# Optimization experiments

Hardware: AMD Instinct MI355X
Metric: run time of the kernel (lower is better)

The kernel has to match this reference:

```python
import jax, jax.numpy as jnp
import numpy as np

B, S, D, F, E, K = 4, 2048, 768, 3072, 8, 2
LB_W, Z_W = 0.01, 0.001


def setup_inputs() -> dict:
    key = jax.random.key(0)
    ks = jax.random.split(key, 6)
    x = jax.random.normal(ks[0], (B, S, D), dtype=jnp.float32)
    Wr = jax.random.truncated_normal(ks[1], -2.0, 2.0, (D, E), dtype=jnp.float32) * 0.02
    W1 = jax.random.normal(ks[2], (E, D, F), dtype=jnp.float32) * (1.0 / np.sqrt(D))
    b1 = jnp.zeros((E, F), dtype=jnp.float32)
    W2 = jax.random.normal(ks[3], (E, F, D), dtype=jnp.float32) * (1.0 / np.sqrt(F))
    b2 = jnp.zeros((E, D), dtype=jnp.float32)
    return {"x": x, "Wr": Wr, "W1": W1, "b1": b1, "W2": W2, "b2": b2}


def reference(x, Wr, W1, b1, W2, b2):
    # Router
    router_logits = jnp.einsum('bsd,de->bse', x, Wr)            # [B,S,E]
    router_probs = jax.nn.softmax(router_logits, axis=-1)
    top_k_probs, top_k_idx = jax.lax.top_k(router_probs, K)     # [B,S,K]
    top_k_probs = top_k_probs / (jnp.sum(top_k_probs, axis=-1, keepdims=True) + 1e-8)

    # Auxiliary losses
    expert_usage = jnp.mean(router_probs, axis=(0, 1))          # [E]
    mean_usage = jnp.mean(expert_usage)
    var_usage = jnp.mean(jnp.square(expert_usage - mean_usage))
    lb_loss = var_usage / (mean_usage * mean_usage + 1e-8) * jnp.float32(E)
    z_loss = jnp.mean(jnp.square(jax.nn.logsumexp(router_logits, axis=-1)))

    # Combine weights per expert: sum over top-k slots assigned to expert e
    one_hot = jax.nn.one_hot(top_k_idx, E, dtype=x.dtype)       # [B,S,K,E]
    combine = jnp.sum(one_hot * top_k_probs[..., None], axis=2) # [B,S,E]

    # Expert FFNs (loop over fixed small E, vectorized over tokens)
    output = jnp.zeros_like(x)
    for e in range(E):
        h = jax.nn.gelu(jnp.einsum('bsd,df->bsf', x, W1[e]) + b1[e], approximate=False)
        y = jnp.einsum('bsf,fd->bsd', h, W2[e]) + b2[e]
        output = output + y * combine[..., e:e + 1]

    aux = {"load_balancing_loss": lb_loss * LB_W, "router_z_loss": z_loss * Z_W}
    return output, aux["load_balancing_loss"], aux["router_z_loss"]
```

## Files before the change

### kernel.cpp

```cpp
#include <hip/hip_runtime.h>
#include <cstdint>
#include <cstddef>

#define B_ 4
#define S_ 2048
#define D_ 768
#define F_ 3072
#define E_ 8
#define NTOK (B_*S_)
#define NASSIGN (NTOK*2)
#define RBLK 256
#define FBLK 32
#define MAXTILE 136

typedef unsigned short u16;
typedef __attribute__((ext_vector_type(8))) __bf16 bf16x8;
typedef __attribute__((ext_vector_type(4))) float f32x4;

__device__ __forceinline__ u16 f2bf(float f) {
    unsigned int u = __builtin_bit_cast(unsigned int, f);
    u += 0x7fffu + ((u >> 16) & 1u);
    return (u16)(u >> 16);
}

__device__ __forceinline__ void async16(const void* g, void* l) {
    __builtin_amdgcn_global_load_lds(
        (const __attribute__((address_space(1))) unsigned int*)g,
        (__attribute__((address_space(3))) unsigned int*)l, 16, 0, 0);
}

__device__ __forceinline__ float gelu_f(float v) {
    float z = v * 0.70710678f;
    float a = fabsf(z);
    float t = __builtin_amdgcn_rcpf(1.0f + 0.3275911f * a);
    float poly = t * (0.254829592f + t * (-0.284496736f + t * (1.421413741f +
                 t * (-1.453152027f + t * 1.061405429f))));
    float e = __expf(-z * z);
    float erf_z = copysignf(1.0f - poly * e, z);
    return 0.5f * v * (1.0f + erf_z);
}

__device__ __forceinline__ int xcd_tile(int xcd, int mloc, int nt, int* ok) {
    int q = nt >> 3, r = nt & 7;
    int cntx = q + (xcd < r ? 1 : 0);
    *ok = (mloc < cntx);
    return xcd * q + (xcd < r ? xcd : r) + mloc;
}

__global__ void k_cvt_x(const float* __restrict__ x, u16* __restrict__ xb) {
    int id = blockIdx.x * 256 + threadIdx.x;
    float4 v = ((const float4*)x)[id];
    ushort4 o;
    o.x = f2bf(v.x); o.y = f2bf(v.y); o.z = f2bf(v.z); o.w = f2bf(v.w);
    ((ushort4*)xb)[id] = o;
}

__global__ __launch_bounds__(256) void k_tcvt(const float* __restrict__ in, u16* __restrict__ out, int R, int C) {
    __shared__ u16 t[64][72];
    int e = blockIdx.z;
    int c0 = blockIdx.x * 64, r0 = blockIdx.y * 64;
    int tid = threadIdx.x;
    int sx = tid & 15;
    int sy = tid >> 4;
    const float* ip = in + (size_t)e * R * C + (size_t)(r0 + sy * 4) * C + c0 + sx * 4;
    float4 v0 = *(const float4*)(ip);
    float4 v1 = *(const float4*)(ip + C);
    float4 v2 = *(const float4*)(ip + 2 * (size_t)C);
    float4 v3 = *(const float4*)(ip + 3 * (size_t)C);
    ushort4 o;
    o.x = f2bf(v0.x); o.y = f2bf(v1.x); o.z = f2bf(v2.x); o.w = f2bf(v3.x);
    *(ushort4*)&t[sx * 4 + 0][sy * 4] = o;
    o.x = f2bf(v0.y); o.y = f2bf(v1.y); o.z = f2bf(v2.y); o.w = f2bf(v3.y);
    *(ushort4*)&t[sx * 4 + 1][sy * 4] = o;
    o.x = f2bf(v0.z); o.y = f2bf(v1.z); o.z = f2bf(v2.z); o.w = f2bf(v3.z);
    *(ushort4*)&t[sx * 4 + 2][sy * 4] = o;
    o.x = f2bf(v0.w); o.y = f2bf(v1.w); o.z = f2bf(v2.w); o.w = f2bf(v3.w);
    *(ushort4*)&t[sx * 4 + 3][sy * 4] = o;
    __syncthreads();
    int od = tid & 7;
    int oc = tid >> 3;
    u16* obase = out + (size_t)e * C * R;
    #pragma unroll
    for (int p = 0; p < 2; p++) {
        int c = oc + p * 32;
        *(uint4*)(obase + (size_t)(c0 + c) * R + r0 + od * 8) = *(const uint4*)&t[c][od * 8];
    }
}

__global__ __launch_bounds__(256) void k_router(
    const float* __restrict__ x, const float* __restrict__ Wr,
    float* __restrict__ usage_part, float* __restrict__ z_part,
    int* __restrict__ hist_part,
    int* __restrict__ tk_idx, float* __restrict__ tk_w)
{
    __shared__ float wrt[E_ * D_];
    __shared__ float s_usage[E_];
    __shared__ float s_z;
    __shared__ int   s_hist[E_];
    int tid = threadIdx.x;
    for (int i = tid; i < E_ * D_; i += 256) {
        int d = i >> 3, e = i & 7;
        wrt[e * D_ + d] = Wr[i];
    }
    if (tid < E_) { s_usage[tid] = 0.f; s_hist[tid] = 0; }
    if (tid == 0) s_z = 0.f;
    __syncthreads();

    int w = tid >> 6, lane = tid & 63;
    float u_acc[E_];
    #pragma unroll
    for (int e = 0; e < E_; e++) u_acc[e] = 0.f;
    float z_acc = 0.f;

    for (int it = 0; it < 8; it++) {
        int tok = blockIdx.x * 32 + it * 4 + w;
        float acc[E_];
        #pragma unroll
        for (int e = 0; e < E_; e++) acc[e] = 0.f;
        const float* xr = x + (size_t)tok * D_;
        for (int d = lane; d < D_; d += 64) {
            float xv = xr[d];
            #pragma unroll
            for (int e = 0; e < E_; e++) acc[e] += xv * wrt[e * D_ + d];
        }
        #pragma unroll
        for (int off = 32; off > 0; off >>= 1) {
            #pragma unroll
            for (int e = 0; e < E_; e++) acc[e] += __shfl_down(acc[e], off);
        }
        if (lane == 0) {
            float m = acc[0];
            #pragma unroll
            for (int e = 1; e < E_; e++) m = fmaxf(m, acc[e]);
            float p[E_], s = 0.f;
            #pragma unroll
            for (int e = 0; e < E_; e++) { p[e] = expf(acc[e] - m); s += p[e]; }
            float inv = 1.f / s;
            #pragma unroll
            for (int e = 0; e < E_; e++) { p[e] *= inv; u_acc[e] += p[e]; }
            float lse = m + logf(s);
            z_acc += lse * lse;
            int i1 = 0;
            for (int e = 1; e < E_; e++) if (p[e] > p[i1]) i1 = e;
            int i2 = -1;
            for (int e = 0; e < E_; e++) {
                if (e == i1) continue;
                if (i2 < 0 || p[e] > p[i2]) i2 = e;
            }
            float denom = p[i1] + p[i2] + 1e-8f;
            tk_idx[tok * 2 + 0] = i1; tk_idx[tok * 2 + 1] = i2;
            tk_w[tok * 2 + 0] = p[i1] / denom;
            tk_w[tok * 2 + 1] = p[i2] / denom;
            atomicAdd(&s_hist[i1], 1); atomicAdd(&s_hist[i2], 1);
        }
    }
    if (lane == 0) {
        #pragma unroll
        for (int e = 0; e < E_; e++) atomicAdd(&s_usage[e], u_acc[e]);
        atomicAdd(&s_z, z_acc);
    }
    __syncthreads();
    if (tid < E_) {
        usage_part[blockIdx.x * E_ + tid] = s_usage[tid];
        hist_part[blockIdx.x * E_ + tid]  = s_hist[tid];
    }
    if (tid == 0) z_part[blockIdx.x] = s_z;
}

__global__ __launch_bounds__(256) void k_finalize(
    const float* __restrict__ usage_part, const float* __restrict__ z_part,
    const int* __restrict__ hist_part,
    int* __restrict__ counts, int* __restrict__ offsets,
    int* __restrict__ cursors,
    int* __restrict__ tile_list,
    float* __restrict__ out_scalars)
{
    __shared__ float s_u[E_];
    __shared__ float s_z;
    __shared__ int   s_h[E_];
    int tid = threadIdx.x;
    if (tid < E_) { s_u[tid] = 0.f; s_h[tid] = 0; cursors[tid] = 0; }
    if (tid == 0) s_z = 0.f;
    __syncthreads();

    float u[E_]; int h[E_];
    #pragma unroll
    for (int e = 0; e < E_; e++) { u[e] = usage_part[tid * E_ + e]; h[e] = hist_part[tid * E_ + e]; }
    float z = z_part[tid];
    #pragma unroll
    for (int off = 32; off > 0; off >>= 1) {
        #pragma unroll
        for (int e = 0; e < E_; e++) {
            u[e] += __shfl_down(u[e], off);
            h[e] += __shfl_down(h[e], off);
        }
        z += __shfl_down(z, off);
    }
    if ((tid & 63) == 0) {
        #pragma unroll
        for (int e = 0; e < E_; e++) { atomicAdd(&s_u[e], u[e]); atomicAdd(&s_h[e], h[e]); }
        atomicAdd(&s_z, z);
    }
    __syncthreads();
    if (tid == 0) {
        int o = 0, nt = 0;
        for (int e = 0; e < E_; e++) {
            int c = s_h[e];
            counts[e] = c; offsets[e] = o; o += c;
            for (int m0 = 0; m0 < c; m0 += 128) tile_list[1 + nt++] = (m0 << 8) | e;
        }
        tile_list[0] = nt;
        float uu[E_], mean = 0.f;
        for (int e = 0; e < E_; e++) { uu[e] = s_u[e] / (float)NTOK; mean += uu[e]; }
        mean /= (float)E_;
        float var = 0.f;
        for (int e = 0; e < E_; e++) { float d = uu[e] - mean; var += d * d; }
        var /= (float)E_;
        out_scalars[0] = var / (mean * mean + 1e-8f) * (float)E_ * 0.01f;
        out_scalars[1] = (s_z / (float)NTOK) * 0.001f;
    }
}

__global__ __launch_bounds__(256) void k_fill(
    const int* __restrict__ tk_idx, const float* __restrict__ tk_w,
    const int* __restrict__ offsets, int* __restrict__ cursors,
    int* __restrict__ assign_token, float* __restrict__ assign_weight)
{
    __shared__ int l_cnt[E_];
    __shared__ int l_base[E_];
    int tid = threadIdx.x;
    if (tid < E_) l_cnt[tid] = 0;
    __syncthreads();
    int t = blockIdx.x * 256 + tid;
    int e0 = tk_idx[t * 2 + 0], e1 = tk_idx[t * 2 + 1];
    int r0 = atomicAdd(&l_cnt[e0], 1);
    int r1 = atomicAdd(&l_cnt[e1], 1);
    __syncthreads();
    if (tid < E_) l_base[tid] = atomicAdd(&cursors[tid], l_cnt[tid]);
    __syncthreads();
    int row0 = offsets[e0] + l_base[e0] + r0;
    int row1 = offsets[e1] + l_base[e1] + r1;
    assign_token[row0] = t; assign_weight[row0] = tk_w[t * 2 + 0];
    assign_token[row1] = t; assign_weight[row1] = tk_w[t * 2 + 1];
}

__global__ __launch_bounds__(256) void k_gemm1(
    const u16* __restrict__ xb, const u16* __restrict__ w1t,
    const float* __restrict__ b1,
    const int* __restrict__ counts, const int* __restrict__ offsets,
    const int* __restrict__ tile_list,
    const int* __restrict__ assign_token, u16* __restrict__ h)
{
    int bid = blockIdx.x;
    int xcd = bid & 7;
    int j = bid >> 3;
    int nx = j / 17;
    int mloc = j % 17;
    int nt = tile_list[0];
    int ok;
    int mt = xcd_tile(xcd, mloc, nt, &ok);
    if (!ok) return;
    int packed = tile_list[1 + mt];
    int e = packed & 0xff;
    int m0 = packed >> 8;
    int cnt = counts[e];
    int off = offsets[e];
    int n0 = nx * 128;

    __shared__ __align__(16) u16 SM[16384];
    char* smb = (char*)SM;

    int tid = threadIdx.x;
    int w = tid >> 6, lane = tid & 63;
    int rA = lane >> 2;
    int colk = ((lane & 3) ^ (rA & 3)) * 8;
    int r0 = (w * 2 + 0) * 16 + rA;
    int r1 = (w * 2 + 1) * 16 + rA;

    int c0b = __builtin_amdgcn_readfirstlane((w * 2 + 0) * 1024);
    int c1b = __builtin_amdgcn_readfirstlane((w * 2 + 1) * 1024);

    int g0 = m0 + r0; if (g0 > cnt - 1) g0 = cnt - 1;
    int g1 = m0 + r1; if (g1 > cnt - 1) g1 = cnt - 1;
    const u16* agp0 = xb + (size_t)assign_token[off + g0] * D_ + colk;
    const u16* agp1 = xb + (size_t)assign_token[off + g1] * D_ + colk;
    const u16* bgp0 = w1t + ((size_t)e * F_ + n0 + r0) * D_ + colk;
    const u16* bgp1 = w1t + ((size_t)e * F_ + n0 + r1) * D_ + colk;

    f32x4 acc[4][4];
    #pragma unroll
    for (int i = 0; i < 4; i++)
        #pragma unroll
        for (int j2 = 0; j2 < 4; j2++) acc[i][j2] = (f32x4){0.f, 0.f, 0.f, 0.f};

    int wm = (w >> 1) * 64, wn = (w & 1) * 64;
    int fm = lane & 15;
    int slot = ((lane >> 4) ^ (fm & 3)) * 8;

    #define STAGE1(buf, kk) do { \
        async16(agp0 + (kk), smb + (buf) * 8192 + c0b); \
        async16(agp1 + (kk), smb + (buf) * 8192 + c1b); \
        async16(bgp0 + (kk), smb + 16384 + (buf) * 8192 + c0b); \
        async16(bgp1 + (kk), smb + 16384 + (buf) * 8192 + c1b); \
    } while (0)
    #define COMPUTE1(buf) do { \
        const u16* Ab = SM + (buf) * 4096; \
        const u16* Bb = SM + 8192 + (buf) * 4096; \
        bf16x8 af[4], bfr[4]; \
        _Pragma("unroll") \
        for (int i = 0; i < 4; i++) af[i] = *(const bf16x8*)&Ab[(wm + i * 16 + fm) * 32 + slot]; \
        _Pragma("unroll") \
        for (int j2 = 0; j2 < 4; j2++) bfr[j2] = *(const bf16x8*)&Bb[(wn + j2 * 16 + fm) * 32 + slot]; \
        _Pragma("unroll") \
        for (int i = 0; i < 4; i++) \
            _Pragma("unroll") \
            for (int j2 = 0; j2 < 4; j2++) \
                acc[i][j2] = __builtin_amdgcn_mfma_f32_16x16x32_bf16(af[i], bfr[j2], acc[i][j2], 0, 0, 0); \
    } while (0)

    STAGE1(0, 0);
    __syncthreads();
    for (int kk = 0; kk < D_; kk += 64) {
        STAGE1(1, kk + 32);
        COMPUTE1(0);
        __syncthreads();
        if (kk + 64 < D_) STAGE1(0, kk + 64);
        COMPUTE1(1);
        __syncthreads();
    }
    #undef STAGE1
    #undef COMPUTE1

    int rbase = (lane >> 4) * 4;
    u16* tb = SM + w * 4096;
    float biasv[4];
    #pragma unroll
    for (int j2 = 0; j2 < 4; j2++) biasv[j2] = b1[e * F_ + n0 + wn + j2 * 16 + fm];
    #pragma unroll
    for (int i = 0; i < 4; i++)
        #pragma unroll
        for (int j2 = 0; j2 < 4; j2++)
            #pragma unroll
            for (int r = 0; r < 4; r++) {
                int m_l = i * 16 + rbase + r;
                int f_l = j2 * 16 + fm;
                u16 q = f2bf(gelu_f(acc[i][j2][r] + biasv[j2]));
                tb[m_l * 64 + ((((f_l >> 3) ^ (m_l & 7)) << 3) | (f_l & 7))] = q;
            }
    __syncthreads();
    #pragma unroll
    for (int s = 0; s < 8; s++) {
        int m_l = s * 8 + (lane >> 3);
        int c = lane & 7;
        uint4 vv = *(const uint4*)&tb[m_l * 64 + ((c ^ (m_l & 7)) << 3)];
        int m = m0 + wm + m_l;
        if (m < cnt)
            *(uint4*)&h[(size_t)(off + m) * F_ + n0 + wn + c * 8] = vv;
    }
}

__global__ __launch_bounds__(256) void k_gemm2(
    const u16* __restrict__ h, const u16* __restrict__ w2t,
    const float* __restrict__ b2,
    const int* __restrict__ counts, const int* __restrict__ offsets,
    const int* __restrict__ tile_list,
    const int* __restrict__ assign_token, const float* __restrict__ assign_weight,
    float* __restrict__ out)
{
    int bid = blockIdx.x;
    int xcd = bid & 7;
    int j = bid >> 3;
    int mloc = j / 12;
    int rem = j % 12;
    int nx = rem % 6;
    int kh = rem / 6;
    int nt = tile_list[0];
    int ok;
    int mt = xcd_tile(xcd, mloc, nt, &ok);
    if (!ok) return;
    int packed = tile_list[1 + mt];
    int e = packed & 0xff;
    int m0 = packed >> 8;
    int cnt = counts[e];
    int off = offsets[e];
    int n0 = nx * 128;
    int kbase = kh * (F_ / 2);
    int kend = kbase + F_ / 2;

    __shared__ __align__(16) u16 SM[16384];
    char* smb = (char*)SM;

    int tid = threadIdx.x;
    int w = tid >> 6, lane = tid & 63;
    int rA = lane >> 2;
    int colk = ((lane & 3) ^ (rA & 3)) * 8;
    int r0 = (w * 2 + 0) * 16 + rA;
    int r1 = (w * 2 + 1) * 16 + rA;

    int c0b = __builtin_amdgcn_readfirstlane((w * 2 + 0) * 1024);
    int c1b = __builtin_amdgcn_readfirstlane((w * 2 + 1) * 1024);

    const u16* agp0 = h + (size_t)(off + m0 + r0) * F_ + colk;
    const u16* agp1 = h + (size_t)(off + m0 + r1) * F_ + colk;
    const u16* bgp0 = w2t + ((size_t)e * D_ + n0 + r0) * F_ + colk;
    const u16* bgp1 = w2t + ((size_t)e * D_ + n0 + r1) * F_ + colk;

    f32x4 acc[4][4];
    #pragma unroll
    for (int i = 0; i < 4; i++)
        #pragma unroll
        for (int j2 = 0; j2 < 4; j2++) acc[i][j2] = (f32x4){0.f, 0.f, 0.f, 0.f};

    int wm = (w >> 1) * 64, wn = (w & 1) * 64;
    int fm = lane & 15;
    int slot = ((lane >> 4) ^ (fm & 3)) * 8;

    #define STAGE2(buf, kk) do { \
        async16(agp0 + (kk), smb + (buf) * 8192 + c0b); \
        async16(agp1 + (kk), smb + (buf) * 8192 + c1b); \
        async16(bgp0 + (kk), smb + 16384 + (buf) * 8192 + c0b); \
        async16(bgp1 + (kk), smb + 16384 + (buf) * 8192 + c1b); \
    } while (0)
    #define COMPUTE2(buf) do { \
        const u16* Ab = SM + (buf) * 4096; \
        const u16* Bb = SM + 8192 + (buf) * 4096; \
        bf16x8 af[4], bfr[4]; \
        _Pragma("unroll") \
        for (int i = 0; i < 4; i++) af[i] = *(const bf16x8*)&Ab[(wm + i * 16 + fm) * 32 + slot]; \
        _Pragma("unroll") \
        for (int j2 = 0; j2 < 4; j2++) bfr[j2] = *(const bf16x8*)&Bb[(wn + j2 * 16 + fm) * 32 + slot]; \
        _Pragma("unroll") \
        for (int i = 0; i < 4; i++) \
            _Pragma("unroll") \
            for (int j2 = 0; j2 < 4; j2++) \
                acc[i][j2] = __builtin_amdgcn_mfma_f32_16x16x32_bf16(af[i], bfr[j2], acc[i][j2], 0, 0, 0); \
    } while (0)

    STAGE2(0, kbase);
    __syncthreads();
    for (int kk = kbase; kk < kend; kk += 64) {
        STAGE2(1, kk + 32);
        COMPUTE2(0);
        __syncthreads();
        if (kk + 64 < kend) STAGE2(0, kk + 64);
        COMPUTE2(1);
        __syncthreads();
    }
    #undef STAGE2
    #undef COMPUTE2

    int rbase = (lane >> 4) * 4;
    float biasv[4];
    #pragma unroll
    for (int j2 = 0; j2 < 4; j2++)
        biasv[j2] = (kh == 0) ? b2[e * D_ + n0 + wn + j2 * 16 + fm] : 0.f;
    #pragma unroll
    for (int i = 0; i < 4; i++)
        #pragma unroll
        for (int r = 0; r < 4; r++) {
            int m = m0 + wm + i * 16 + rbase + r;
            if (m < cnt) {
                int t = assign_token[off + m];
                float wg = assign_weight[off + m];
                float* orow = out + (size_t)t * D_ + n0 + wn + fm;
                #pragma unroll
                for (int j2 = 0; j2 < 4; j2++)
                    unsafeAtomicAdd(orow + j2 * 16, (acc[i][j2][r] + biasv[j2]) * wg);
            }
        }
}

extern "C" void kernel_launch(void* const* d_in, const int* in_sizes, int n_in,
                              void* d_out, int out_size, void* d_ws, size_t ws_size,
                              hipStream_t stream)
{
    const float* x  = (const float*)d_in[0];
    const float* Wr = (const float*)d_in[1];
    const float* W1 = (const float*)d_in[2];
    const float* b1 = (const float*)d_in[3];
    const float* W2 = (const float*)d_in[4];
    const float* b2 = (const float*)d_in[5];
    float* out = (float*)d_out;

    char* base = (char*)d_ws;
    size_t o = 0;
    auto alloc = [&](size_t bytes) {
        char* r = base + o;
        o += (bytes + 255) & ~(size_t)255;
        return r;
    };
    int*   counts        = (int*)  alloc(E_ * 4);
    int*   cursors       = (int*)  alloc(E_ * 4);
    int*   offsets       = (int*)  alloc(E_ * 4);
    int*   tile_list     = (int*)  alloc(256 * 4);
    float* usage_part    = (float*)alloc((size_t)RBLK * E_ * 4);
    float* z_part        = (float*)alloc((size_t)RBLK * 4);
    int*   hist_part     = (int*)  alloc((size_t)RBLK * E_ * 4);
    int*   tk_idx        = (int*)  alloc((size_t)NTOK * 2 * 4);
    float* tk_w          = (float*)alloc((size_t)NTOK * 2 * 4);
    int*   assign_token  = (int*)  alloc((size_t)NASSIGN * 4);
    float* assign_weight = (float*)alloc((size_t)NASSIGN * 4);
    u16*   xb            = (u16*)  alloc((size_t)NTOK * D_ * 2);
    u16*   w1t           = (u16*)  alloc((size_t)E_ * F_ * D_ * 2);
    u16*   w2t           = (u16*)  alloc((size_t)E_ * D_ * F_ * 2);
    u16*   hbuf          = (u16*)  alloc((size_t)(NASSIGN + 128) * F_ * 2);

    hipMemsetAsync(d_out, 0, (size_t)out_size * 4, stream);
    k_cvt_x<<<dim3(NTOK * D_ / 1024), dim3(256), 0, stream>>>(x, xb);
    k_tcvt<<<dim3(F_ / 64, D_ / 64, E_), dim3(256), 0, stream>>>(W1, w1t, D_, F_);
    k_tcvt<<<dim3(D_ / 64, F_ / 64, E_), dim3(256), 0, stream>>>(W2, w2t, F_, D_);
    k_router<<<dim3(RBLK), dim3(256), 0, stream>>>(x, Wr, usage_part, z_part, hist_part, tk_idx, tk_w);
    k_finalize<<<dim3(1), dim3(256), 0, stream>>>(usage_part, z_part, hist_part, counts, offsets,
                                                  cursors, tile_list, out + (size_t)NTOK * D_);
    k_fill<<<dim3(FBLK), dim3(256), 0, stream>>>(tk_idx, tk_w, offsets, cursors, assign_token, assign_weight);
    k_gemm1<<<dim3(8 * 17 * (F_ / 128)), dim3(256), 0, stream>>>(xb, w1t, b1, counts, offsets, tile_list,
                                                                 assign_token, hbuf);
    k_gemm2<<<dim3(8 * 17 * (D_ / 128) * 2), dim3(256), 0, stream>>>(hbuf, w2t, b2, counts, offsets, tile_list,
                                                                     assign_token, assign_weight, out);
}
```

Baseline: 616.7 us.

## Triple-buffer GEMM K-loops with vmcnt waits and drop split-K in gemm2

Both expert GEMMs move from a double-buffered LDS loop with full __syncthreads to a three-stage ring that waits with s_waitcnt vmcnt(4) plus a barrier, so two tiles of loads stay in flight during each MFMA step. gemm2 no longer splits the K dimension in two: each block covers all of F, which halves the grid and halves the atomic adds into the output. Bias, token indices and routing weights are preloaded before the main loop. The cost is more LDS per block (48KB), which may lower occupancy, and fewer blocks in gemm2 to fill the GPU.

```diff
diff --git a/kernel.cpp b/kernel.cpp
--- a/kernel.cpp
+++ b/kernel.cpp
@@ -11,7 +11,6 @@
 #define NASSIGN (NTOK*2)
 #define RBLK 256
 #define FBLK 32
-#define MAXTILE 136
 
 typedef unsigned short u16;
 typedef __attribute__((ext_vector_type(8))) __bf16 bf16x8;
@@ -28,6 +27,17 @@
         (const __attribute__((address_space(1))) unsigned int*)g,
         (__attribute__((address_space(3))) unsigned int*)l, 16, 0, 0);
 }
+
+#define PWAIT4 do { \
+    asm volatile("s_waitcnt vmcnt(4) lgkmcnt(0)" ::: "memory"); \
+    __builtin_amdgcn_s_barrier(); \
+    asm volatile("" ::: "memory"); \
+} while (0)
+#define PWAIT0 do { \
+    asm volatile("s_waitcnt vmcnt(0) lgkmcnt(0)" ::: "memory"); \
+    __builtin_amdgcn_s_barrier(); \
+    asm volatile("" ::: "memory"); \
+} while (0)
 
 __device__ __forceinline__ float gelu_f(float v) {
     float z = v * 0.70710678f;
@@ -267,7 +277,7 @@
     int off = offsets[e];
     int n0 = nx * 128;
 
-    __shared__ __align__(16) u16 SM[16384];
+    __shared__ __align__(16) u16 SM[24576];
     char* smb = (char*)SM;
 
     int tid = threadIdx.x;
@@ -297,15 +307,24 @@
     int fm = lane & 15;
     int slot = ((lane >> 4) ^ (fm & 3)) * 8;
 
-    #define STAGE1(buf, kk) do { \
-        async16(agp0 + (kk), smb + (buf) * 8192 + c0b); \
-        async16(agp1 + (kk), smb + (buf) * 8192 + c1b); \
-        async16(bgp0 + (kk), smb + 16384 + (buf) * 8192 + c0b); \
-        async16(bgp1 + (kk), smb + 16384 + (buf) * 8192 + c1b); \
+    float biasv[4];
+    #pragma unroll
+    for (int j2 = 0; j2 < 4; j2++) {
+        biasv[j2] = b1[e * F_ + n0 + wn + j2 * 16 + fm];
+        asm volatile("" : "+v"(biasv[j2]));
+    }
+
+    #define STAGE1(p, kk) do { \
+        char* Ad = smb + (p) * 8192; \
+        char* Bd = smb + 24576 + (p) * 8192; \
+        async16(agp0 + (kk), Ad + c0b); \
+        async16(agp1 + (kk), Ad + c1b); \
+        async16(bgp0 + (kk), Bd + c0b); \
+        async16(bgp1 + (kk), Bd + c1b); \
     } while (0)
-    #define COMPUTE1(buf) do { \
-        const u16* Ab = SM + (buf) * 4096; \
-        const u16* Bb = SM + 8192 + (buf) * 4096; \
+    #define COMPUTE1(p) do { \
+        const u16* Ab = SM + (p) * 4096; \
+        const u16* Bb = SM + 12288 + (p) * 4096; \
         bf16x8 af[4], bfr[4]; \
         _Pragma("unroll") \
         for (int i = 0; i < 4; i++) af[i] = *(const bf16x8*)&Ab[(wm + i * 16 + fm) * 32 + slot]; \
@@ -319,23 +338,22 @@
     } while (0)
 
     STAGE1(0, 0);
-    __syncthreads();
-    for (int kk = 0; kk < D_; kk += 64) {
-        STAGE1(1, kk + 32);
-        COMPUTE1(0);
-        __syncthreads();
-        if (kk + 64 < D_) STAGE1(0, kk + 64);
-        COMPUTE1(1);
-        __syncthreads();
-    }
+    STAGE1(1, 32);
+    int q0 = 0, q1 = 1, q2 = 2;
+    for (int t = 0; t < 22; ++t) {
+        PWAIT4;
+        STAGE1(q2, (t + 2) * 32);
+        COMPUTE1(q0);
+        int tmp = q0; q0 = q1; q1 = q2; q2 = tmp;
+    }
+    PWAIT4; COMPUTE1(q0);
+    PWAIT0; COMPUTE1(q1);
     #undef STAGE1
     #undef COMPUTE1
+    __syncthreads();
 
     int rbase = (lane >> 4) * 4;
     u16* tb = SM + w * 4096;
-    float biasv[4];
-    #pragma unroll
-    for (int j2 = 0; j2 < 4; j2++) biasv[j2] = b1[e * F_ + n0 + wn + j2 * 16 + fm];
     #pragma unroll
     for (int i = 0; i < 4; i++)
         #pragma unroll
@@ -370,10 +388,8 @@
     int bid = blockIdx.x;
     int xcd = bid & 7;
     int j = bid >> 3;
-    int mloc = j / 12;
-    int rem = j % 12;
-    int nx = rem % 6;
-    int kh = rem / 6;
+    int nx = j % 6;
+    int mloc = j / 6;
     int nt = tile_list[0];
     int ok;
     int mt = xcd_tile(xcd, mloc, nt, &ok);
@@ -384,10 +400,8 @@
     int cnt = counts[e];
     int off = offsets[e];
     int n0 = nx * 128;
-    int kbase = kh * (F_ / 2);
-    int kend = kbase + F_ / 2;
-
-    __shared__ __align__(16) u16 SM[16384];
+
+    __shared__ __align__(16) u16 SM[24576];
     char* smb = (char*)SM;
 
     int tid = threadIdx.x;
@@ -414,16 +428,38 @@
     int wm = (w >> 1) * 64, wn = (w & 1) * 64;
     int fm = lane & 15;
     int slot = ((lane >> 4) ^ (fm & 3)) * 8;
-
-    #define STAGE2(buf, kk) do { \
-        async16(agp0 + (kk), smb + (buf) * 8192 + c0b); \
-        async16(agp1 + (kk), smb + (buf) * 8192 + c1b); \
-        async16(bgp0 + (kk), smb + 16384 + (buf) * 8192 + c0b); \
-        async16(bgp1 + (kk), smb + 16384 + (buf) * 8192 + c1b); \
+    int rbase = (lane >> 4) * 4;
+
+    float biasv[4];
+    #pragma unroll
+    for (int j2 = 0; j2 < 4; j2++) {
+        biasv[j2] = b2[e * D_ + n0 + wn + j2 * 16 + fm];
+        asm volatile("" : "+v"(biasv[j2]));
+    }
+    int tokv[4][4]; float wgtv[4][4];
+    #pragma unroll
+    for (int i = 0; i < 4; i++)
+        #pragma unroll
+        for (int r = 0; r < 4; r++) {
+            int m = m0 + wm + i * 16 + rbase + r;
+            int mr = (m < cnt) ? m : (cnt - 1);
+            tokv[i][r] = assign_token[off + mr];
+            wgtv[i][r] = assign_weight[off + mr];
+            asm volatile("" : "+v"(tokv[i][r]));
+            asm volatile("" : "+v"(wgtv[i][r]));
+        }
+
+    #define STAGE2(p, kk) do { \
+        char* Ad = smb + (p) * 8192; \
+        char* Bd = smb + 24576 + (p) * 8192; \
+        async16(agp0 + (kk), Ad + c0b); \
+        async16(agp1 + (kk), Ad + c1b); \
+        async16(bgp0 + (kk), Bd + c0b); \
+        async16(bgp1 + (kk), Bd + c1b); \
     } while (0)
-    #define COMPUTE2(buf) do { \
-        const u16* Ab = SM + (buf) * 4096; \
-        const u16* Bb = SM + 8192 + (buf) * 4096; \
+    #define COMPUTE2(p) do { \
+        const u16* Ab = SM + (p) * 4096; \
+        const u16* Bb = SM + 12288 + (p) * 4096; \
         bf16x8 af[4], bfr[4]; \
         _Pragma("unroll") \
         for (int i = 0; i < 4; i++) af[i] = *(const bf16x8*)&Ab[(wm + i * 16 + fm) * 32 + slot]; \
@@ -436,33 +472,28 @@
                 acc[i][j2] = __builtin_amdgcn_mfma_f32_16x16x32_bf16(af[i], bfr[j2], acc[i][j2], 0, 0, 0); \
     } while (0)
 
-    STAGE2(0, kbase);
-    __syncthreads();
-    for (int kk = kbase; kk < kend; kk += 64) {
-        STAGE2(1, kk + 32);
-        COMPUTE2(0);
-        __syncthreads();
-        if (kk + 64 < kend) STAGE2(0, kk + 64);
-        COMPUTE2(1);
-        __syncthreads();
-    }
+    STAGE2(0, 0);
+    STAGE2(1, 32);
+    int q0 = 0, q1 = 1, q2 = 2;
+    for (int t = 0; t < 94; ++t) {
+        PWAIT4;
+        STAGE2(q2, (t + 2) * 32);
+        COMPUTE2(q0);
+        int tmp = q0; q0 = q1; q1 = q2; q2 = tmp;
+    }
+    PWAIT4; COMPUTE2(q0);
+    PWAIT0; COMPUTE2(q1);
     #undef STAGE2
     #undef COMPUTE2
 
-    int rbase = (lane >> 4) * 4;
-    float biasv[4];
-    #pragma unroll
-    for (int j2 = 0; j2 < 4; j2++)
-        biasv[j2] = (kh == 0) ? b2[e * D_ + n0 + wn + j2 * 16 + fm] : 0.f;
     #pragma unroll
     for (int i = 0; i < 4; i++)
         #pragma unroll
         for (int r = 0; r < 4; r++) {
             int m = m0 + wm + i * 16 + rbase + r;
             if (m < cnt) {
-                int t = assign_token[off + m];
-                float wg = assign_weight[off + m];
-                float* orow = out + (size_t)t * D_ + n0 + wn + fm;
+                float* orow = out + (size_t)tokv[i][r] * D_ + n0 + wn + fm;
+                float wg = wgtv[i][r];
                 #pragma unroll
                 for (int j2 = 0; j2 < 4; j2++)
                     unsafeAtomicAdd(orow + j2 * 16, (acc[i][j2][r] + biasv[j2]) * wg);
@@ -515,6 +546,6 @@
     k_fill<<<dim3(FBLK), dim3(256), 0, stream>>>(tk_idx, tk_w, offsets, cursors, assign_token, assign_weight);
     k_gemm1<<<dim3(8 * 17 * (F_ / 128)), dim3(256), 0, stream>>>(xb, w1t, b1, counts, offsets, tile_list,
                                                                  assign_token, hbuf);
-    k_gemm2<<<dim3(8 * 17 * (D_ / 128) * 2), dim3(256), 0, stream>>>(hbuf, w2t, b2, counts, offsets, tile_list,
-                                                                     assign_token, assign_weight, out);
-}
+    k_gemm2<<<dim3(8 * 17 * (D_ / 128)), dim3(256), 0, stream>>>(hbuf, w2t, b2, counts, offsets, tile_list,
+                                                                 assign_token, assign_weight, out);
+}
```

Result: faster. 529.7 us (-14.1%).
